# Kernel optimization log

Measured on AMD Instinct MI355X. Metric: run time of the kernel, lower is better.

Reference implementation:

```python
import jax, jax.numpy as jnp
import numpy as np

WINDOW_SIZES = (1, 2, 3)
COV_DIM = 128
MEM_DIM = 128
BATCH = 8192


def setup_inputs() -> dict:
    rng = np.random.default_rng(0)
    sizes = rng.integers(16, 64, size=BATCH)
    total = int(sizes.sum())  # ~327k tokens
    key = jax.random.key(0)
    ks = jax.random.split(key, 10)
    s = 0.05
    inp = {
        "x": jax.random.normal(ks[0], (total, COV_DIM), jnp.float32),
        "sizes": jnp.asarray(sizes, jnp.int32),
    }
    for i, w in enumerate(WINDOW_SIZES):
        inp[f"conv_w{i}"] = jax.random.normal(ks[1 + 2 * i], (MEM_DIM, COV_DIM, w), jnp.float32) * s
        inp[f"conv_b{i}"] = jax.random.normal(ks[2 + 2 * i], (MEM_DIM,), jnp.float32) * s
    inp["lin_w"] = jax.random.normal(ks[7], (MEM_DIM, len(WINDOW_SIZES) * MEM_DIM), jnp.float32) * s
    inp["lin_b"] = jax.random.normal(ks[8], (MEM_DIM,), jnp.float32) * s
    return inp


def _temporal_conv(x, w, b):
    # x: [T, C], w: [M, C, k] -> [T-k+1, M]  (valid 1D conv, as nn.Conv1d)
    y = jax.lax.conv_general_dilated(
        x.T[None],  # [1, C, T]
        w,
        window_strides=(1,),
        padding="VALID",
        dimension_numbers=("NCH", "OIH", "NCH"),
    )[0]  # [M, L]
    return y.T + b


def _dmax(h, sizes, window_size, batch):
    # Ragged per-segment max over dim 0 of the concatenated conv output.
    # Segment i covers rows [off_i, off_i + sizes[i] - window_size + 1) where
    # off_i is the exclusive cumsum of sizes (DMax advances start_idx by sizes[i]).
    L = h.shape[0]  # total - window_size + 1
    cum = jnp.cumsum(sizes)  # [B], inclusive
    p = jnp.arange(L)
    seg = jnp.searchsorted(cum, p, side="right")  # segment owning row p
    valid = p + (window_size - 1) < cum[seg]  # within sizes[i]-w+1 prefix
    seg = jnp.where(valid, seg, batch)  # dump invalid rows in a trash segment
    return jax.ops.segment_max(h, seg, num_segments=batch + 1)[:batch]


def reference(x, sizes, conv_w0, conv_b0, conv_w1, conv_b1, conv_w2, conv_b2, lin_w, lin_b):
    batch = sizes.shape[0]
    convs = ((conv_w0, conv_b0), (conv_w1, conv_b1), (conv_w2, conv_b2))
    pools = []
    for wsz, (cw, cb) in zip(WINDOW_SIZES, convs):
        h = jax.nn.relu(_temporal_conv(x, cw, cb))  # [T-w+1, M]
        pools.append(_dmax(h, sizes, wsz, batch))  # [B, M]
    concat = jnp.concatenate(pools, axis=1)  # [B, 3M]
    return jnp.tanh(concat @ lin_w.T + lin_b)  # [B, M]
```

## Files before the change

### kernel.cpp

```cpp
#include <hip/hip_runtime.h>
#include <hip/hip_bf16.h>

typedef __bf16 bf16x8 __attribute__((ext_vector_type(8)));
typedef __bf16 bf16x4 __attribute__((ext_vector_type(4)));
typedef float  f32x4  __attribute__((ext_vector_type(4)));

#define MFMA16(a, b, c) __builtin_amdgcn_mfma_f32_16x16x32_bf16((a), (b), (c), 0, 0, 0)

__global__ void k_prep(const int* __restrict__ sizes, int* __restrict__ offsets,
                       const float* __restrict__ w0, const float* __restrict__ w1,
                       const float* __restrict__ w2, const float* __restrict__ lw,
                       __bf16* __restrict__ Wpack,
                       __bf16* __restrict__ Lhi, __bf16* __restrict__ Llo) {
  const int bid = blockIdx.x, t = threadIdx.x;
  if (bid == 240) {
    __shared__ int part[256];
    const int base = t * 32;
    int v[32];
    int s = 0;
#pragma unroll
    for (int i = 0; i < 32; ++i) { v[i] = sizes[base + i]; s += v[i]; }
    part[t] = s;
    __syncthreads();
    for (int d = 1; d < 256; d <<= 1) {
      int add = (t >= d) ? part[t - d] : 0;
      __syncthreads();
      part[t] += add;
      __syncthreads();
    }
    int run = (t == 0) ? 0 : part[t - 1];
#pragma unroll
    for (int i = 0; i < 32; ++i) { offsets[base + i] = run; run += v[i]; }
  } else if (bid < 48) {
    const int nt = bid, sl = nt >> 3, f = nt & 7;
    const int kt = t >> 6, lane = t & 63;
    const float* src; int kw, jj;
    if      (sl == 0) { src = w0; kw = 1; jj = 0; }
    else if (sl == 1) { src = w1; kw = 2; jj = 0; }
    else if (sl == 2) { src = w1; kw = 2; jj = 1; }
    else if (sl == 3) { src = w2; kw = 3; jj = 0; }
    else if (sl == 4) { src = w2; kw = 3; jj = 1; }
    else              { src = w2; kw = 3; jj = 2; }
    const int feat  = f * 16 + (lane & 15);
    const int cbase = kt * 32 + ((lane >> 4) << 3);
    __bf16* dst = Wpack + ((((nt * 4 + kt) << 6) + lane) << 3);
#pragma unroll
    for (int j = 0; j < 8; ++j)
      dst[j] = (__bf16)src[(feat * 128 + cbase + j) * kw + jj];
  } else {
    const int idx = (bid - 48) * 256 + t;
    const int j = idx & 7, lane = (idx >> 3) & 63, rest = idx >> 9;
    const int kt = rest % 12, nt = rest / 12;
    const int o = nt * 16 + (lane & 15);
    const int q = kt * 32 + ((lane >> 4) << 3) + j;
    const float v = lw[o * 384 + q];
    const __bf16 hi = (__bf16)v;
    Lhi[idx] = hi;
    Llo[idx] = (__bf16)(v - (float)hi);
  }
}

__global__ __launch_bounds__(256, 4)
void k_conv(const float* __restrict__ x, const int* __restrict__ sizes,
            const int* __restrict__ offsets,
            const float* __restrict__ cb0, const float* __restrict__ cb1,
            const float* __restrict__ cb2,
            const bf16x8* __restrict__ Wpack,
            __bf16* __restrict__ Phi, __bf16* __restrict__ Plo) {
  __shared__ __bf16 xh[66 * 136];
  const int b = blockIdx.x;
  const int s = sizes[b];
  const long off = offsets[b];
  const int t = threadIdx.x;
  const int MT = (s + 15) >> 4;

  {
    const int quads = s << 5;
    float4 v[8];
#pragma unroll
    for (int i = 0; i < 8; ++i) {
      const int qi = t + (i << 8);
      if (qi < quads) {
        const int r = qi >> 5, c = (qi & 31) << 2;
        v[i] = *(const float4*)(x + (off + r) * 128 + c);
      }
    }
#pragma unroll
    for (int i = 0; i < 8; ++i) {
      const int qi = t + (i << 8);
      if (qi < quads) {
        const int r = qi >> 5, c = (qi & 31) << 2;
        bf16x4 h; h[0] = (__bf16)v[i].x; h[1] = (__bf16)v[i].y;
                  h[2] = (__bf16)v[i].z; h[3] = (__bf16)v[i].w;
        *(bf16x4*)&xh[r * 136 + c] = h;
      }
    }
    const int zend = MT * 16 + 2;
    const int c = (t & 31) << 2;
    for (int r = s + (t >> 5); r < zend; r += 8)
      *(bf16x4*)&xh[r * 136 + c] =
          bf16x4{(__bf16)0.f, (__bf16)0.f, (__bf16)0.f, (__bf16)0.f};
  }
  __syncthreads();

  const int wid = t >> 6, lane = t & 63;
  const int lo16 = lane & 15, g16 = lane >> 4;

#pragma unroll
  for (int fi = 0; fi < 2; ++fi) {
    const int ft = wid + (fi << 2);
    const int feat = ft * 16 + lo16;

    f32x4 acc[4][3];
#pragma unroll
    for (int mt = 0; mt < 4; ++mt)
#pragma unroll
      for (int p = 0; p < 3; ++p)
        acc[mt][p] = f32x4{0.f, 0.f, 0.f, 0.f};

#pragma unroll
    for (int kt = 0; kt < 4; ++kt) {
      bf16x8 bf[6];
#pragma unroll
      for (int sl = 0; sl < 6; ++sl)
        bf[sl] = Wpack[(((sl * 8 + ft) * 4 + kt) << 6) + lane];
#pragma unroll
      for (int mt = 0; mt < 4; ++mt) {
        if (mt < MT) {
          const __bf16* ap = &xh[(mt * 16 + lo16) * 136 + kt * 32 + (g16 << 3)];
          const bf16x8 A0 = *(const bf16x8*)ap;
          const bf16x8 A1 = *(const bf16x8*)(ap + 136);
          const bf16x8 A2 = *(const bf16x8*)(ap + 272);
          acc[mt][0] = MFMA16(A0, bf[0], acc[mt][0]);
          acc[mt][1] = MFMA16(A0, bf[1], acc[mt][1]);
          acc[mt][1] = MFMA16(A1, bf[2], acc[mt][1]);
          acc[mt][2] = MFMA16(A0, bf[3], acc[mt][2]);
          acc[mt][2] = MFMA16(A1, bf[4], acc[mt][2]);
          acc[mt][2] = MFMA16(A2, bf[5], acc[mt][2]);
        }
      }
    }

    float m1 = -1e30f, m2 = -1e30f, m3 = -1e30f;
#pragma unroll
    for (int mt = 0; mt < 4; ++mt) {
      if (mt >= MT) continue;
#pragma unroll
      for (int v = 0; v < 4; ++v) {
        const int lrow = mt * 16 + g16 * 4 + v;
        if (lrow < s)     m1 = fmaxf(m1, acc[mt][0][v]);
        if (lrow < s - 1) m2 = fmaxf(m2, acc[mt][1][v]);
        if (lrow < s - 2) m3 = fmaxf(m3, acc[mt][2][v]);
      }
    }
    m1 = fmaxf(m1, __shfl_xor(m1, 16)); m1 = fmaxf(m1, __shfl_xor(m1, 32));
    m2 = fmaxf(m2, __shfl_xor(m2, 16)); m2 = fmaxf(m2, __shfl_xor(m2, 32));
    m3 = fmaxf(m3, __shfl_xor(m3, 16)); m3 = fmaxf(m3, __shfl_xor(m3, 32));
    if (g16 == 0) {
      const float p1 = fmaxf(m1 + cb0[feat], 0.f);
      const float p2 = fmaxf(m2 + cb1[feat], 0.f);
      const float p3 = fmaxf(m3 + cb2[feat], 0.f);
      const __bf16 h1 = (__bf16)p1, h2 = (__bf16)p2, h3 = (__bf16)p3;
      const long row = (long)b * 384;
      Phi[row + feat]       = h1;
      Plo[row + feat]       = (__bf16)(p1 - (float)h1);
      Phi[row + 128 + feat] = h2;
      Plo[row + 128 + feat] = (__bf16)(p2 - (float)h2);
      Phi[row + 256 + feat] = h3;
      Plo[row + 256 + feat] = (__bf16)(p3 - (float)h3);
    }
  }
}

__global__ __launch_bounds__(256, 4)
void k_lin(const __bf16* __restrict__ Phi, const __bf16* __restrict__ Plo,
           const bf16x8* __restrict__ Lhi, const bf16x8* __restrict__ Llo,
           const float* __restrict__ lb, float* __restrict__ out) {
  __shared__ __bf16 ph[16 * 392];
  __shared__ __bf16 pl[16 * 392];
  const int blk = blockIdx.x, t = threadIdx.x;
  const long rbase = (long)blk * 16;
#pragma unroll
  for (int i = 0; i < 3; ++i) {
    const int ci = t + (i << 8);
    const int r = ci / 48, cc = ci % 48;
    *(int4*)&ph[r * 392 + (cc << 3)] = *(const int4*)&Phi[(rbase + r) * 384 + (cc << 3)];
    *(int4*)&pl[r * 392 + (cc << 3)] = *(const int4*)&Plo[(rbase + r) * 384 + (cc << 3)];
  }
  __syncthreads();
  const int wid = t >> 6, lane = t & 63;
  const int lo16 = lane & 15, g = lane >> 4;
#pragma unroll
  for (int ni = 0; ni < 2; ++ni) {
    const int nt = wid + (ni << 2);
    f32x4 acc = f32x4{0.f, 0.f, 0.f, 0.f};
#pragma unroll
    for (int kt = 0; kt < 12; ++kt) {
      const bf16x8 bh = Lhi[((nt * 12 + kt) << 6) + lane];
      const bf16x8 bl = Llo[((nt * 12 + kt) << 6) + lane];
      const int aoff = lo16 * 392 + kt * 32 + (g << 3);
      const bf16x8 ah = *(const bf16x8*)&ph[aoff];
      const bf16x8 al = *(const bf16x8*)&pl[aoff];
      acc = MFMA16(ah, bh, acc);
      acc = MFMA16(al, bh, acc);
      acc = MFMA16(ah, bl, acc);
    }
    const int o = nt * 16 + lo16;
    const float bias = lb[o];
#pragma unroll
    for (int v = 0; v < 4; ++v) {
      const int r = g * 4 + v;
      const float val = acc[v] + bias;
      out[(rbase + r) * 128 + o] = 1.f - 2.f / (__expf(2.f * val) + 1.f);
    }
  }
}

extern "C" void kernel_launch(void* const* d_in, const int* in_sizes, int n_in,
                              void* d_out, int out_size, void* d_ws, size_t ws_size,
                              hipStream_t stream) {
  const float* x   = (const float*)d_in[0];
  const int* sizes = (const int*)d_in[1];
  const float* w0  = (const float*)d_in[2];
  const float* cb0 = (const float*)d_in[3];
  const float* w1  = (const float*)d_in[4];
  const float* cb1 = (const float*)d_in[5];
  const float* w2  = (const float*)d_in[6];
  const float* cb2 = (const float*)d_in[7];
  const float* lw  = (const float*)d_in[8];
  const float* lb  = (const float*)d_in[9];

  char* ws = (char*)d_ws;
  size_t o = 0;
  int*    offsets = (int*)ws;                 o += 32768;
  __bf16* Wpack   = (__bf16*)(ws + o);        o += 196608;
  __bf16* Lhi     = (__bf16*)(ws + o);        o += 98304;
  __bf16* Llo     = (__bf16*)(ws + o);        o += 98304;
  __bf16* Phi     = (__bf16*)(ws + o);        o += 8192L * 384 * 2;
  __bf16* Plo     = (__bf16*)(ws + o);        o += 8192L * 384 * 2;

  k_prep<<<241, 256, 0, stream>>>(sizes, offsets, w0, w1, w2, lw, Wpack, Lhi, Llo);
  k_conv<<<8192, 256, 0, stream>>>(x, sizes, offsets, cb0, cb1, cb2,
                                   (const bf16x8*)Wpack, Phi, Plo);
  k_lin<<<512, 256, 0, stream>>>(Phi, Plo, (const bf16x8*)Lhi,
                                 (const bf16x8*)Llo, lb, (float*)d_out);
}
```

Baseline: 324.9 us.

## Make conv kernel persistent with register-resident weights and double-buffered segment loads

The conv kernel becomes persistent: 256 blocks of 512 threads each process 32 segments in sequence. Each of the 8 waves keeps its feature tile's conv weights in registers for the whole run, and the next segment's x rows are prefetched into registers and written to a second LDS buffer while the current segment's MFMAs run. LDS uses an XOR swizzle in place of padding to avoid bank conflicts. This removes the repeated weight reloads and the per-block launch and load latency, but gives only 256 blocks (one wave of 8 waves per CU at most), uses heavy register pressure, and adds a per-segment barrier.

```diff
diff --git a/kernel.cpp b/kernel.cpp
--- a/kernel.cpp
+++ b/kernel.cpp
@@ -60,56 +60,89 @@
   }
 }
 
-__global__ __launch_bounds__(256, 4)
+#define SPB 32
+
+__global__ __launch_bounds__(512, 2)
 void k_conv(const float* __restrict__ x, const int* __restrict__ sizes,
             const int* __restrict__ offsets,
             const float* __restrict__ cb0, const float* __restrict__ cb1,
             const float* __restrict__ cb2,
             const bf16x8* __restrict__ Wpack,
             __bf16* __restrict__ Phi, __bf16* __restrict__ Plo) {
-  __shared__ __bf16 xh[66 * 136];
-  const int b = blockIdx.x;
-  const int s = sizes[b];
-  const long off = offsets[b];
+  __shared__ __align__(16) __bf16 xs[2][66 * 128];
   const int t = threadIdx.x;
-  const int MT = (s + 15) >> 4;
-
-  {
-    const int quads = s << 5;
-    float4 v[8];
-#pragma unroll
-    for (int i = 0; i < 8; ++i) {
-      const int qi = t + (i << 8);
-      if (qi < quads) {
-        const int r = qi >> 5, c = (qi & 31) << 2;
-        v[i] = *(const float4*)(x + (off + r) * 128 + c);
-      }
-    }
-#pragma unroll
-    for (int i = 0; i < 8; ++i) {
-      const int qi = t + (i << 8);
-      if (qi < quads) {
-        const int r = qi >> 5, c = (qi & 31) << 2;
-        bf16x4 h; h[0] = (__bf16)v[i].x; h[1] = (__bf16)v[i].y;
-                  h[2] = (__bf16)v[i].z; h[3] = (__bf16)v[i].w;
-        *(bf16x4*)&xh[r * 136 + c] = h;
-      }
-    }
-    const int zend = MT * 16 + 2;
-    const int c = (t & 31) << 2;
-    for (int r = s + (t >> 5); r < zend; r += 8)
-      *(bf16x4*)&xh[r * 136 + c] =
-          bf16x4{(__bf16)0.f, (__bf16)0.f, (__bf16)0.f, (__bf16)0.f};
-  }
-  __syncthreads();
-
   const int wid = t >> 6, lane = t & 63;
   const int lo16 = lane & 15, g16 = lane >> 4;
 
-#pragma unroll
-  for (int fi = 0; fi < 2; ++fi) {
-    const int ft = wid + (fi << 2);
-    const int feat = ft * 16 + lo16;
+  bf16x8 wf[6][4];
+#pragma unroll
+  for (int sl = 0; sl < 6; ++sl)
+#pragma unroll
+    for (int kt = 0; kt < 4; ++kt)
+      wf[sl][kt] = Wpack[(((sl * 8 + wid) * 4 + kt) << 6) + lane];
+
+  const int xr0 = lo16 & 7, xr1 = (lo16 + 1) & 7, xr2 = (lo16 + 2) & 7;
+  const int seg0 = blockIdx.x * SPB;
+
+  int s_cur = sizes[seg0];
+  const long o_cur = offsets[seg0];
+
+  {
+    const int uend = (((s_cur + 15) >> 4) * 16 + 2) << 4;
+#pragma unroll
+    for (int k = 0; k < 3; ++k) {
+      const int u = t + (k << 9);
+      if (u < uend) {
+        const int r = u >> 4, g = u & 15;
+        bf16x8 h;
+        if (r < s_cur) {
+          const float* p = x + (o_cur + r) * 128 + (g << 3);
+          const float4 a = *(const float4*)p;
+          const float4 b = *(const float4*)(p + 4);
+          h[0] = (__bf16)a.x; h[1] = (__bf16)a.y; h[2] = (__bf16)a.z; h[3] = (__bf16)a.w;
+          h[4] = (__bf16)b.x; h[5] = (__bf16)b.y; h[6] = (__bf16)b.z; h[7] = (__bf16)b.w;
+        } else {
+#pragma unroll
+          for (int j = 0; j < 8; ++j) h[j] = (__bf16)0.f;
+        }
+        *(bf16x8*)&xs[0][r * 128 + ((g ^ (r & 7)) << 3)] = h;
+      }
+    }
+  }
+  __syncthreads();
+
+  int cur = 0;
+  int s_nn = sizes[seg0 + 1];
+  int o_nn = offsets[seg0 + 1];
+
+  for (int i = 0; i < SPB; ++i) {
+    const int seg = seg0 + i;
+    const int s = s_cur;
+    const int MT = (s + 15) >> 4;
+
+    const int s_nxt = s_nn;
+    const long o_nxt = o_nn;
+    float4 va[3], vb[3];
+    bool act[3] = {false, false, false}, lv[3] = {false, false, false};
+    if (i + 1 < SPB) {
+      const int uend = (((s_nxt + 15) >> 4) * 16 + 2) << 4;
+#pragma unroll
+      for (int k = 0; k < 3; ++k) {
+        const int u = t + (k << 9);
+        const int r = u >> 4, g = u & 15;
+        act[k] = (u < uend);
+        lv[k] = act[k] && (r < s_nxt);
+        if (lv[k]) {
+          const float* p = x + (o_nxt + r) * 128 + (g << 3);
+          va[k] = *(const float4*)p;
+          vb[k] = *(const float4*)(p + 4);
+        }
+      }
+      if (i + 2 < SPB) {
+        s_nn = sizes[seg0 + i + 2];
+        o_nn = offsets[seg0 + i + 2];
+      }
+    }
 
     f32x4 acc[4][3];
 #pragma unroll
@@ -118,50 +151,71 @@
       for (int p = 0; p < 3; ++p)
         acc[mt][p] = f32x4{0.f, 0.f, 0.f, 0.f};
 
+    const __bf16* xb = xs[cur];
 #pragma unroll
     for (int kt = 0; kt < 4; ++kt) {
-      bf16x8 bf[6];
-#pragma unroll
-      for (int sl = 0; sl < 6; ++sl)
-        bf[sl] = Wpack[(((sl * 8 + ft) * 4 + kt) << 6) + lane];
+      const int gg = kt * 4 + g16;
 #pragma unroll
       for (int mt = 0; mt < 4; ++mt) {
         if (mt < MT) {
-          const __bf16* ap = &xh[(mt * 16 + lo16) * 136 + kt * 32 + (g16 << 3)];
-          const bf16x8 A0 = *(const bf16x8*)ap;
-          const bf16x8 A1 = *(const bf16x8*)(ap + 136);
-          const bf16x8 A2 = *(const bf16x8*)(ap + 272);
-          acc[mt][0] = MFMA16(A0, bf[0], acc[mt][0]);
-          acc[mt][1] = MFMA16(A0, bf[1], acc[mt][1]);
-          acc[mt][1] = MFMA16(A1, bf[2], acc[mt][1]);
-          acc[mt][2] = MFMA16(A0, bf[3], acc[mt][2]);
-          acc[mt][2] = MFMA16(A1, bf[4], acc[mt][2]);
-          acc[mt][2] = MFMA16(A2, bf[5], acc[mt][2]);
-        }
-      }
-    }
-
-    float m1 = -1e30f, m2 = -1e30f, m3 = -1e30f;
+          const int rb = mt * 16 + lo16;
+          const bf16x8 A0 = *(const bf16x8*)&xb[(rb    ) * 128 + ((gg ^ xr0) << 3)];
+          const bf16x8 A1 = *(const bf16x8*)&xb[(rb + 1) * 128 + ((gg ^ xr1) << 3)];
+          const bf16x8 A2 = *(const bf16x8*)&xb[(rb + 2) * 128 + ((gg ^ xr2) << 3)];
+          acc[mt][0] = MFMA16(A0, wf[0][kt], acc[mt][0]);
+          acc[mt][1] = MFMA16(A0, wf[1][kt], acc[mt][1]);
+          acc[mt][2] = MFMA16(A0, wf[3][kt], acc[mt][2]);
+          acc[mt][1] = MFMA16(A1, wf[2][kt], acc[mt][1]);
+          acc[mt][2] = MFMA16(A1, wf[4][kt], acc[mt][2]);
+          acc[mt][2] = MFMA16(A2, wf[5][kt], acc[mt][2]);
+        }
+      }
+    }
+
+    if (i + 1 < SPB) {
+#pragma unroll
+      for (int k = 0; k < 3; ++k) {
+        if (act[k]) {
+          const int u = t + (k << 9);
+          const int r = u >> 4, g = u & 15;
+          bf16x8 h;
+          if (lv[k]) {
+            h[0] = (__bf16)va[k].x; h[1] = (__bf16)va[k].y;
+            h[2] = (__bf16)va[k].z; h[3] = (__bf16)va[k].w;
+            h[4] = (__bf16)vb[k].x; h[5] = (__bf16)vb[k].y;
+            h[6] = (__bf16)vb[k].z; h[7] = (__bf16)vb[k].w;
+          } else {
+#pragma unroll
+            for (int j = 0; j < 8; ++j) h[j] = (__bf16)0.f;
+          }
+          *(bf16x8*)&xs[cur ^ 1][r * 128 + ((g ^ (r & 7)) << 3)] = h;
+        }
+      }
+    }
+
+    float m1 = -3e38f, m2 = -3e38f, m3 = -3e38f;
 #pragma unroll
     for (int mt = 0; mt < 4; ++mt) {
-      if (mt >= MT) continue;
-#pragma unroll
-      for (int v = 0; v < 4; ++v) {
-        const int lrow = mt * 16 + g16 * 4 + v;
-        if (lrow < s)     m1 = fmaxf(m1, acc[mt][0][v]);
-        if (lrow < s - 1) m2 = fmaxf(m2, acc[mt][1][v]);
-        if (lrow < s - 2) m3 = fmaxf(m3, acc[mt][2][v]);
+      if (mt < MT) {
+#pragma unroll
+        for (int v = 0; v < 4; ++v) {
+          const int lrow = mt * 16 + g16 * 4 + v;
+          if (lrow < s)     m1 = fmaxf(m1, acc[mt][0][v]);
+          if (lrow < s - 1) m2 = fmaxf(m2, acc[mt][1][v]);
+          if (lrow < s - 2) m3 = fmaxf(m3, acc[mt][2][v]);
+        }
       }
     }
     m1 = fmaxf(m1, __shfl_xor(m1, 16)); m1 = fmaxf(m1, __shfl_xor(m1, 32));
     m2 = fmaxf(m2, __shfl_xor(m2, 16)); m2 = fmaxf(m2, __shfl_xor(m2, 32));
     m3 = fmaxf(m3, __shfl_xor(m3, 16)); m3 = fmaxf(m3, __shfl_xor(m3, 32));
     if (g16 == 0) {
+      const int feat = wid * 16 + lo16;
       const float p1 = fmaxf(m1 + cb0[feat], 0.f);
       const float p2 = fmaxf(m2 + cb1[feat], 0.f);
       const float p3 = fmaxf(m3 + cb2[feat], 0.f);
       const __bf16 h1 = (__bf16)p1, h2 = (__bf16)p2, h3 = (__bf16)p3;
-      const long row = (long)b * 384;
+      const long row = (long)seg * 384;
       Phi[row + feat]       = h1;
       Plo[row + feat]       = (__bf16)(p1 - (float)h1);
       Phi[row + 128 + feat] = h2;
@@ -169,6 +223,10 @@
       Phi[row + 256 + feat] = h3;
       Plo[row + 256 + feat] = (__bf16)(p3 - (float)h3);
     }
+
+    __syncthreads();
+    s_cur = s_nxt;
+    cur ^= 1;
   }
 }
 
@@ -240,8 +298,8 @@
   __bf16* Plo     = (__bf16*)(ws + o);        o += 8192L * 384 * 2;
 
   k_prep<<<241, 256, 0, stream>>>(sizes, offsets, w0, w1, w2, lw, Wpack, Lhi, Llo);
-  k_conv<<<8192, 256, 0, stream>>>(x, sizes, offsets, cb0, cb1, cb2,
-                                   (const bf16x8*)Wpack, Phi, Plo);
+  k_conv<<<256, 512, 0, stream>>>(x, sizes, offsets, cb0, cb1, cb2,
+                                  (const bf16x8*)Wpack, Phi, Plo);
   k_lin<<<512, 256, 0, stream>>>(Phi, Plo, (const bf16x8*)Lhi,
                                  (const bf16x8*)Llo, lb, (float*)d_out);
 }
```

New measurement: 331.0 us. No clear change (+1.9%).
